# Optimization experiments

Hardware: AMD Instinct MI355X
Metric: run time of the kernel (lower is better)

## Reference

```python
import jax, jax.numpy as jnp
import numpy as np

B, T, E, H = 2, 4096, 1024, 16
SEGS = (256, 512, 1024, 2048, 4096)
DILS = (1, 2, 4, 8, 16)
NEG = -1e8  # torchscale uses -1e8 for uncovered / masked lse entries


def setup_inputs() -> dict:
    key = jax.random.key(0)
    ks = jax.random.split(key, 5)
    sc = 0.02
    zb = jnp.zeros((E,), jnp.float32)
    return {
        "x": jax.random.normal(ks[0], (B, T, E), jnp.float32),
        "wq": jax.random.normal(ks[1], (E, E), jnp.float32) * sc,
        "bq": zb,
        "wk": jax.random.normal(ks[2], (E, E), jnp.float32) * sc,
        "bk": zb,
        "wv": jax.random.normal(ks[3], (E, E), jnp.float32) * sc,
        "bv": zb,
        "wo": jax.random.normal(ks[4], (E, E), jnp.float32) * sc,
        "bo": zb,
    }


def _scale_attn(q, k, v, w, r):
    # One LongNet scale: segment length w, dilation ratio r.
    # Head group g = head // (H//r) attends to in-segment positions p with p % r == g
    # (torchscale dense_to_sparse diagonal over (r1, r2)).
    Bq, Tq, Hq, d = q.shape
    n, s, hp = Tq // w, w // r, Hq // r  # segments, sparse length, heads per group

    def gather(x):
        # [B,T,H,d] -> segments [B,n,w,H,d]; split w=(s,r1) (p=l*r+r1) and H=(r2,hp);
        # keep diagonal r1 == r2.
        x = x.reshape(Bq, n, s, r, r, hp, d)
        x = jnp.diagonal(x, axis1=3, axis2=4)          # [B,n,s,hp,d,r]
        return jnp.moveaxis(x, -1, 3).reshape(Bq, n, s, Hq, d)

    qs, ks_, vs = gather(q), gather(k), gather(v)
    scores = jnp.einsum('bnqhd,bnkhd->bnhqk', qs, ks_)
    mask = jnp.tril(jnp.ones((s, s), dtype=bool))       # causal within sparse segment
    scores = jnp.where(mask, scores, NEG)
    lse = jax.scipy.special.logsumexp(scores, axis=-1)  # [B,n,h,q]
    out = jnp.einsum('bnhqk,bnkhd->bnqhd', jax.nn.softmax(scores, axis=-1), vs)

    # Scatter back to dense positions (sparse_to_dense): uncovered -> out 0, lse -1e8.
    eye = jnp.eye(r, dtype=out.dtype)
    out_g = out.reshape(Bq, n, s, r, hp, d)                               # heads as (g, hp)
    dense = jnp.einsum('bnsghd,pg->bnspghd', out_g, eye).reshape(Bq, Tq, Hq, d)
    lse_g = jnp.transpose(lse, (0, 1, 3, 2)).reshape(Bq, n, s, r, hp)     # [B,n,s,g,hp]
    lse_d = jnp.where(eye[:, :, None] > 0, lse_g[:, :, :, None, :, :], NEG)
    return dense, lse_d.reshape(Bq, Tq, Hq)


def reference(x, wq, bq, wk, bk, wv, bv, wo, bo):
    d = E // H
    q = (x @ wq + bq).reshape(B, T, H, d) * (d ** -0.5)
    k = (x @ wk + bk).reshape(B, T, H, d)
    v = (x @ wv + bv).reshape(B, T, H, d)
    outs, lses = [], []
    for w_, r_ in zip(SEGS, DILS):
        o, l = _scale_attn(q, k, v, w_, r_)
        outs.append(o)
        lses.append(l)
    # Merge scales with softmax over per-scale log-sum-exp (dense-attention equivalence).
    wgt = jax.nn.softmax(jnp.stack(lses), axis=0)[..., None]  # [S,B,T,H,1]
    y = jnp.sum(jnp.stack(outs) * wgt, axis=0).reshape(B, T, E)
    return y @ wo + bo
```

## Files before the change

kernel.cpp:

```cpp
#include <hip/hip_runtime.h>
#include <hip/hip_bf16.h>

typedef __bf16 bf16_t;
typedef __bf16 bf16x8 __attribute__((ext_vector_type(8)));
typedef __bf16 bf16x4 __attribute__((ext_vector_type(4)));
typedef float f32x4 __attribute__((ext_vector_type(4)));
typedef int vint4 __attribute__((ext_vector_type(4)));

#define AS1 __attribute__((address_space(1)))
#define AS3 __attribute__((address_space(3)))

constexpr int B_ = 2, T_ = 4096, E_ = 1024, H_ = 16;
constexpr int M_ = B_ * T_;

__device__ constexpr size_t OB_OFF[5]  = {0, 8388608, 12582912, 14680064, 15728640};
__device__ constexpr size_t LSE_OFF[5] = {0, 131072, 196608, 229376, 245760};
constexpr size_t OB_TOTAL  = 16252928;
constexpr size_t LSE_TOTAL = 253952;

__global__ __launch_bounds__(256) void cvt_f32_bf16(const float* __restrict__ in,
                                                    bf16_t* __restrict__ out) {
  int i = (blockIdx.x * 256 + threadIdx.x) * 4;
  const float4 v = *(const float4*)(in + i);
  bf16x4 o;
  o[0] = (bf16_t)v.x; o[1] = (bf16_t)v.y; o[2] = (bf16_t)v.z; o[3] = (bf16_t)v.w;
  *(bf16x4*)(out + i) = o;
}

__global__ __launch_bounds__(256) void cvt_transpose_w(
    const float* __restrict__ w0, const float* __restrict__ w1,
    const float* __restrict__ w2, const float* __restrict__ w3,
    bf16_t* __restrict__ o0, bf16_t* __restrict__ o1,
    bf16_t* __restrict__ o2, bf16_t* __restrict__ o3) {
  __shared__ float tile[32][33];
  const float* src; bf16_t* dst;
  switch (blockIdx.z) {
    case 0: src = w0; dst = o0; break;
    case 1: src = w1; dst = o1; break;
    case 2: src = w2; dst = o2; break;
    default: src = w3; dst = o3; break;
  }
  const int n0 = blockIdx.x * 32, k0 = blockIdx.y * 32;
  const int tx = threadIdx.x & 31, ty = threadIdx.x >> 5;
#pragma unroll
  for (int i = 0; i < 32; i += 8)
    tile[ty + i][tx] = src[(size_t)(k0 + ty + i) * E_ + n0 + tx];
  __syncthreads();
#pragma unroll
  for (int i = 0; i < 32; i += 8)
    dst[(size_t)(n0 + ty + i) * E_ + k0 + tx] = (bf16_t)tile[tx][ty + i];
}

template <bool OUT_BF16, bool QKV>
__global__ __launch_bounds__(512, 1) void gemm_dp(
    const bf16_t* __restrict__ A, const bf16_t* __restrict__ BT,
    const float* __restrict__ bias0, const float* __restrict__ bias1,
    const float* __restrict__ bias2, void* __restrict__ Cout) {
  constexpr int K = E_;
  constexpr int NT = K / 64;
  __shared__ bf16_t Sm[73728];

  const int tid = threadIdx.x;
  const int lane = tid & 63;
  const int wid = tid >> 6;
  const int wm = wid >> 1, wn = wid & 1;
  const int lc = lane & 15, lg = lane >> 4;
  const int bm = blockIdx.x;
  int bn = blockIdx.y;

  const float* bias = bias0;
  float scale = 1.0f;
  void* outp = Cout;
  const bf16_t* Bt = BT;
  if (QKV) {
    const int which = bn >> 3;
    bn &= 7;
    bias = (which == 0) ? bias0 : (which == 1) ? bias1 : bias2;
    scale = (which == 0) ? 0.125f : 1.0f;
    outp = (void*)((bf16_t*)Cout + (size_t)which * M_ * E_);
    Bt += (size_t)which * E_ * E_;
  }

  const int srow = tid >> 3;
  const int schunk = (tid & 7) ^ (srow & 7);
  const bf16_t* Ag = A + (size_t)(bm * 256 + srow) * K + schunk * 8;
  const bf16_t* Bg = Bt + (size_t)(bn * 128 + srow) * K + schunk * 8;

  auto stA = [&](int kt, int bu) {
#pragma unroll
    for (int l = 0; l < 4; ++l)
      __builtin_amdgcn_global_load_lds(
          (const AS1 void*)(Ag + (size_t)(l * 64) * K + kt * 64),
          (AS3 void*)(Sm + bu * 16384 + l * 4096 + tid * 8), 16, 0, 0);
  };
  auto stB = [&](int kt, int bu) {
#pragma unroll
    for (int l = 0; l < 2; ++l)
      __builtin_amdgcn_global_load_lds(
          (const AS1 void*)(Bg + (size_t)(l * 64) * K + kt * 64),
          (AS3 void*)(Sm + 49152 + bu * 8192 + l * 4096 + tid * 8), 16, 0, 0);
  };

  const int sl0 = ((lg) ^ (lc & 7)) * 8;
  const int sl1 = ((4 + lg) ^ (lc & 7)) * 8;

  f32x4 acc[4][4] = {};

  stA(0, 0); stB(0, 0);
  stA(1, 1); stB(1, 1);

  for (int kt = 0; kt < NT; ++kt) {
    const int bc = kt % 3;
    if (kt + 2 < NT) {
      const int bs = (kt + 2) % 3;
      stA(kt + 2, bs); stB(kt + 2, bs);
      asm volatile("s_waitcnt vmcnt(12)" ::: "memory");
    } else if (kt + 1 < NT) {
      asm volatile("s_waitcnt vmcnt(6)" ::: "memory");
    } else {
      asm volatile("s_waitcnt vmcnt(0)" ::: "memory");
    }
    __builtin_amdgcn_s_barrier();
    asm volatile("" ::: "memory");

    const int ab = bc * 16384 + (wm * 64 + lc) * 64;
    const int bb = 49152 + bc * 8192 + (wn * 64 + lc) * 64;
    bf16x8 afr[4][2], bfr[4][2];
#pragma unroll
    for (int i = 0; i < 4; ++i) {
      afr[i][0] = *(const bf16x8*)&Sm[ab + i * 1024 + sl0];
      afr[i][1] = *(const bf16x8*)&Sm[ab + i * 1024 + sl1];
    }
#pragma unroll
    for (int j = 0; j < 4; ++j) {
      bfr[j][0] = *(const bf16x8*)&Sm[bb + j * 1024 + sl0];
      bfr[j][1] = *(const bf16x8*)&Sm[bb + j * 1024 + sl1];
    }
#pragma unroll
    for (int i = 0; i < 4; ++i)
#pragma unroll
      for (int j = 0; j < 4; ++j) {
        acc[i][j] = __builtin_amdgcn_mfma_f32_16x16x32_bf16(afr[i][0], bfr[j][0], acc[i][j], 0, 0, 0);
        acc[i][j] = __builtin_amdgcn_mfma_f32_16x16x32_bf16(afr[i][1], bfr[j][1], acc[i][j], 0, 0, 0);
      }
    asm volatile("" ::: "memory");
    __builtin_amdgcn_s_barrier();
  }

#pragma unroll
  for (int i = 0; i < 4; ++i) {
    const int row = bm * 256 + wm * 64 + i * 16 + lg * 4;
#pragma unroll
    for (int j = 0; j < 4; ++j) {
      const int col = bn * 128 + wn * 64 + j * 16 + lc;
      const float bv = bias[col];
#pragma unroll
      for (int rg = 0; rg < 4; ++rg) {
        const float v = (acc[i][j][rg] + bv) * scale;
        if (OUT_BF16)
          ((bf16_t*)outp)[(size_t)(row + rg) * E_ + col] = (bf16_t)v;
        else
          ((float*)outp)[(size_t)(row + rg) * E_ + col] = v;
      }
    }
  }
}

__global__ __launch_bounds__(512, 4) void attn_inst(
    const bf16_t* __restrict__ Q, const bf16_t* __restrict__ K,
    const bf16_t* __restrict__ V, bf16_t* __restrict__ Ob,
    float* __restrict__ Lse) {
  __shared__ alignas(16) bf16_t Ks[256][72];
  __shared__ alignas(16) bf16_t Vt[64][264];
  __shared__ alignas(16) bf16_t Pw[8][16][40];

  const int bid = blockIdx.x;
  int s, ibase;
  if (bid < 512)      { s = 0; ibase = 0; }
  else if (bid < 768) { s = 1; ibase = 512; }
  else if (bid < 896) { s = 2; ibase = 768; }
  else if (bid < 960) { s = 3; ibase = 896; }
  else                { s = 4; ibase = 960; }
  const int inst = bid - ibase;
  const int h = inst & 15;
  const int nseg_log = 4 - s;
  const int seg = (inst >> 4) & ((1 << nseg_log) - 1);
  const int b = inst >> (4 + nseg_log);
  const int g = h >> (4 - s);

  const int t = threadIdx.x;
  const int lane = t & 63;
  const int wv = t >> 6;
  const int lc = lane & 15;
  const int lg = lane >> 4;

  {
    const int row = t >> 1, ch = (t & 1) * 32;
    const int tk = ((seg * 256 + row) << s) + g;
    const size_t off = ((size_t)b * T_ + tk) * E_ + h * 64 + ch;
    const bf16_t* Kg = K + off;
    const bf16_t* Vg = V + off;
#pragma unroll
    for (int j = 0; j < 4; ++j)
      *(bf16x8*)&Ks[row][ch + j * 8] = *(const bf16x8*)(Kg + j * 8);
#pragma unroll
    for (int j = 0; j < 4; ++j) {
      bf16x8 va = *(const bf16x8*)(Vg + j * 8);
#pragma unroll
      for (int e = 0; e < 8; ++e) Vt[ch + j * 8 + e][row] = va[e];
    }
  }
  __syncthreads();

  const size_t rowbase = (size_t)(b * H_ + h) * (T_ >> s) + seg * 256;

#pragma unroll
  for (int sel = 0; sel < 2; ++sel) {
    const int tile = sel ? (15 - wv) : wv;
    const int q = tile * 16 + lc;

    const int tq = ((seg * 256 + q) << s) + g;
    const bf16_t* Qg = Q + ((size_t)b * T_ + tq) * E_ + h * 64 + lg * 8;
    bf16x8 qfrag0 = *(const bf16x8*)(Qg);
    bf16x8 qfrag1 = *(const bf16x8*)(Qg + 32);

    float m = -INFINITY, Z = 0.0f;
    f32x4 Oa[4] = {};

    const int nkb = tile / 4 + 1;
    const int diag = tile / 4;
    for (int kb = 0; kb < nkb; ++kb) {
      f32x4 sacc[4] = {};
      __builtin_amdgcn_s_setprio(1);
#pragma unroll
      for (int kt = 0; kt < 4; ++kt) {
        bf16x8 kf0 = *(const bf16x8*)&Ks[kb * 64 + kt * 16 + lc][lg * 8];
        bf16x8 kf1 = *(const bf16x8*)&Ks[kb * 64 + kt * 16 + lc][32 + lg * 8];
        sacc[kt] = __builtin_amdgcn_mfma_f32_16x16x32_bf16(kf0, qfrag0, sacc[kt], 0, 0, 0);
        sacc[kt] = __builtin_amdgcn_mfma_f32_16x16x32_bf16(kf1, qfrag1, sacc[kt], 0, 0, 0);
      }
      __builtin_amdgcn_s_setprio(0);
      if (kb == diag) {
#pragma unroll
        for (int kt = 0; kt < 4; ++kt)
#pragma unroll
          for (int rg = 0; rg < 4; ++rg)
            if (kb * 64 + kt * 16 + lg * 4 + rg > q) sacc[kt][rg] = -1e30f;
      }
      float pm = -1e30f;
#pragma unroll
      for (int kt = 0; kt < 4; ++kt) {
        pm = fmaxf(pm, fmaxf(fmaxf(sacc[kt][0], sacc[kt][1]),
                             fmaxf(sacc[kt][2], sacc[kt][3])));
      }
      pm = fmaxf(pm, __shfl_xor(pm, 16));
      pm = fmaxf(pm, __shfl_xor(pm, 32));
      const float nm = fmaxf(m, pm);
      const float crr = __expf(m - nm);
      m = nm;
      float psum = 0.0f;
      bf16x4 pv[4];
#pragma unroll
      for (int kt = 0; kt < 4; ++kt)
#pragma unroll
        for (int rg = 0; rg < 4; ++rg) {
          const float p = __expf(sacc[kt][rg] - nm);
          psum += p;
          pv[kt][rg] = (bf16_t)p;
        }
      psum += __shfl_xor(psum, 16);
      psum += __shfl_xor(psum, 32);
      Z = Z * crr + psum;
#pragma unroll
      for (int dt = 0; dt < 4; ++dt)
#pragma unroll
        for (int rg = 0; rg < 4; ++rg) Oa[dt][rg] *= crr;
#pragma unroll
      for (int hf = 0; hf < 2; ++hf) {
        *(bf16x4*)&Pw[wv][lc][lg * 4]      = pv[hf * 2 + 0];
        *(bf16x4*)&Pw[wv][lc][16 + lg * 4] = pv[hf * 2 + 1];
        bf16x8 pb = *(const bf16x8*)&Pw[wv][lc][lg * 8];
        __builtin_amdgcn_s_setprio(1);
#pragma unroll
        for (int dt = 0; dt < 4; ++dt) {
          bf16x8 vf = *(const bf16x8*)&Vt[dt * 16 + lc][(kb * 2 + hf) * 32 + lg * 8];
          Oa[dt] = __builtin_amdgcn_mfma_f32_16x16x32_bf16(vf, pb, Oa[dt], 0, 0, 0);
        }
        __builtin_amdgcn_s_setprio(0);
      }
    }

    const float lse = m + __logf(Z);
    const float iZ = 1.0f / Z;
    bf16_t* orow = Ob + OB_OFF[s] + (rowbase + q) * 64 + lg * 4;
#pragma unroll
    for (int dt = 0; dt < 4; ++dt) {
      bf16x4 ov;
      ov[0] = (bf16_t)(Oa[dt][0] * iZ);
      ov[1] = (bf16_t)(Oa[dt][1] * iZ);
      ov[2] = (bf16_t)(Oa[dt][2] * iZ);
      ov[3] = (bf16_t)(Oa[dt][3] * iZ);
      *(bf16x4*)(orow + dt * 16) = ov;
    }
    if (lg == 0) Lse[LSE_OFF[s] + rowbase + q] = lse;
  }
}

__global__ __launch_bounds__(256) void attn_merge(const bf16_t* __restrict__ Ob,
                                                  const float* __restrict__ Lse,
                                                  bf16_t* __restrict__ Y) {
  const int gtid = blockIdx.x * 256 + threadIdx.x;
  const int d8 = gtid & 7;
  const int h = (gtid >> 3) & 15;
  const int tt = (gtid >> 7) & (T_ - 1);
  const int b = gtid >> 19;

  float m = -INFINITY, S = 0.0f;
  float acc[8];
#pragma unroll
  for (int j = 0; j < 8; ++j) acc[j] = 0.0f;

#pragma unroll
  for (int s = 0; s < 5; ++s) {
    const int r = 1 << s;
    const int g = h >> (4 - s);
    if ((tt & (r - 1)) != g) continue;
    const size_t idx = (size_t)(b * H_ + h) * (T_ >> s) + (tt >> s);
    const float lse = Lse[LSE_OFF[s] + idx];
    const bf16x8 ov = *(const bf16x8*)(Ob + OB_OFF[s] + idx * 64 + d8 * 8);
    const float nM = fmaxf(m, lse);
    const float a = __expf(m - nM);
    const float e = __expf(lse - nM);
#pragma unroll
    for (int j = 0; j < 8; ++j) acc[j] = acc[j] * a + (float)ov[j] * e;
    S = S * a + e;
    m = nM;
  }

  const float invS = 1.0f / S;
  bf16x8 o;
#pragma unroll
  for (int j = 0; j < 8; ++j) o[j] = (bf16_t)(acc[j] * invS);
  *(bf16x8*)(Y + (size_t)gtid * 8) = o;
}

extern "C" void kernel_launch(void* const* d_in, const int* in_sizes, int n_in,
                              void* d_out, int out_size, void* d_ws, size_t ws_size,
                              hipStream_t stream) {
  (void)in_sizes; (void)n_in; (void)out_size; (void)ws_size;
  const float* x  = (const float*)d_in[0];
  const float* wq = (const float*)d_in[1];
  const float* bq = (const float*)d_in[2];
  const float* wk = (const float*)d_in[3];
  const float* bk = (const float*)d_in[4];
  const float* wv = (const float*)d_in[5];
  const float* bv = (const float*)d_in[6];
  const float* wo = (const float*)d_in[7];
  const float* bo = (const float*)d_in[8];

  char* p = (char*)d_ws;
  auto take = [&](size_t bytes) {
    char* q = p;
    p += (bytes + 255) & ~(size_t)255;
    return (void*)q;
  };
  bf16_t* wq_t = (bf16_t*)take((size_t)E_ * E_ * 2);
  bf16_t* wk_t = (bf16_t*)take((size_t)E_ * E_ * 2);
  bf16_t* wv_t = (bf16_t*)take((size_t)E_ * E_ * 2);
  bf16_t* wo_t = (bf16_t*)take((size_t)E_ * E_ * 2);
  bf16_t* xb   = (bf16_t*)take((size_t)M_ * E_ * 2);
  bf16_t* qb   = (bf16_t*)take((size_t)M_ * E_ * 2);
  bf16_t* kbuf = (bf16_t*)take((size_t)M_ * E_ * 2);
  bf16_t* vbuf = (bf16_t*)take((size_t)M_ * E_ * 2);
  bf16_t* yb   = (bf16_t*)take((size_t)M_ * E_ * 2);
  bf16_t* Ob   = (bf16_t*)take(OB_TOTAL * 2);
  float*  Lse  = (float*)take(LSE_TOTAL * 4);
  (void)wk_t; (void)wv_t;

  cvt_f32_bf16<<<M_ * E_ / 1024, 256, 0, stream>>>(x, xb);
  cvt_transpose_w<<<dim3(32, 32, 4), 256, 0, stream>>>(wq, wk, wv, wo, wq_t, wk_t, wv_t, wo_t);

  gemm_dp<true, true><<<dim3(M_ / 256, 24), 512, 0, stream>>>(
      xb, wq_t, bq, bk, bv, qb);

  attn_inst<<<992, 512, 0, stream>>>(qb, kbuf, vbuf, Ob, Lse);

  attn_merge<<<M_ * E_ / 8 / 256, 256, 0, stream>>>(Ob, Lse, yb);

  gemm_dp<false, false><<<dim3(M_ / 256, 8), 512, 0, stream>>>(
      yb, wo_t, bo, bo, bo, d_out);
}
```

Before: 138.0 us.

## Shrink GEMM tiles, fold log2e into Q scale, add lazy softmax rescaling

Replaces the 256x128 triple-buffered GEMM with a simpler 128x128 tile kernel of 256 threads and no prefetching, allowing up to 4 blocks per CU instead of one large block. Folds log2(e) into the Q scale so attention and merge use exp2/log2 instead of exp/log. Adds a wave-uniform threshold check that skips the running-max rescale of the accumulators when the new block max stays within a bound. The GEMM loses its software pipeline, and the lazy rescale lets exponent values grow before renormalisation.

```diff
diff --git a/kernel.cpp b/kernel.cpp
--- a/kernel.cpp
+++ b/kernel.cpp
@@ -52,18 +52,17 @@
 }
 
 template <bool OUT_BF16, bool QKV>
-__global__ __launch_bounds__(512, 1) void gemm_dp(
+__global__ __launch_bounds__(256, 4) void gemm_bt(
     const bf16_t* __restrict__ A, const bf16_t* __restrict__ BT,
     const float* __restrict__ bias0, const float* __restrict__ bias1,
-    const float* __restrict__ bias2, void* __restrict__ Cout) {
+    const float* __restrict__ bias2, void* __restrict__ Cout, float qscale) {
   constexpr int K = E_;
-  constexpr int NT = K / 64;
-  __shared__ bf16_t Sm[73728];
-
+  __shared__ bf16_t As[128 * 64];
+  __shared__ bf16_t Bs[128 * 64];
   const int tid = threadIdx.x;
   const int lane = tid & 63;
-  const int wid = tid >> 6;
-  const int wm = wid >> 1, wn = wid & 1;
+  const int wave = tid >> 6;
+  const int wm = wave >> 1, wn = wave & 1;
   const int lc = lane & 15, lg = lane >> 4;
   const int bm = blockIdx.x;
   int bn = blockIdx.y;
@@ -76,80 +75,53 @@
     const int which = bn >> 3;
     bn &= 7;
     bias = (which == 0) ? bias0 : (which == 1) ? bias1 : bias2;
-    scale = (which == 0) ? 0.125f : 1.0f;
+    scale = (which == 0) ? qscale : 1.0f;
     outp = (void*)((bf16_t*)Cout + (size_t)which * M_ * E_);
     Bt += (size_t)which * E_ * E_;
   }
 
-  const int srow = tid >> 3;
-  const int schunk = (tid & 7) ^ (srow & 7);
-  const bf16_t* Ag = A + (size_t)(bm * 256 + srow) * K + schunk * 8;
-  const bf16_t* Bg = Bt + (size_t)(bn * 128 + srow) * K + schunk * 8;
-
-  auto stA = [&](int kt, int bu) {
-#pragma unroll
-    for (int l = 0; l < 4; ++l)
+  f32x4 acc[4][4] = {};
+
+  const int lrow = tid >> 3;
+  const int schunk = (tid & 7) ^ (lrow & 7);
+  const bf16_t* Ag = A + (size_t)(bm * 128 + lrow) * K + schunk * 8;
+  const bf16_t* Bg = Bt + (size_t)(bn * 128 + lrow) * K + schunk * 8;
+
+  const int sl0 = ((0 * 4 + lg) ^ (lc & 7)) * 8;
+  const int sl1 = ((1 * 4 + lg) ^ (lc & 7)) * 8;
+
+  for (int k0 = 0; k0 < K; k0 += 64) {
+    __syncthreads();
+#pragma unroll
+    for (int p = 0; p < 4; ++p) {
       __builtin_amdgcn_global_load_lds(
-          (const AS1 void*)(Ag + (size_t)(l * 64) * K + kt * 64),
-          (AS3 void*)(Sm + bu * 16384 + l * 4096 + tid * 8), 16, 0, 0);
-  };
-  auto stB = [&](int kt, int bu) {
-#pragma unroll
-    for (int l = 0; l < 2; ++l)
+          (const AS1 void*)(Ag + (size_t)(p * 32) * K + k0),
+          (AS3 void*)(As + p * 2048 + tid * 8), 16, 0, 0);
       __builtin_amdgcn_global_load_lds(
-          (const AS1 void*)(Bg + (size_t)(l * 64) * K + kt * 64),
-          (AS3 void*)(Sm + 49152 + bu * 8192 + l * 4096 + tid * 8), 16, 0, 0);
-  };
-
-  const int sl0 = ((lg) ^ (lc & 7)) * 8;
-  const int sl1 = ((4 + lg) ^ (lc & 7)) * 8;
-
-  f32x4 acc[4][4] = {};
-
-  stA(0, 0); stB(0, 0);
-  stA(1, 1); stB(1, 1);
-
-  for (int kt = 0; kt < NT; ++kt) {
-    const int bc = kt % 3;
-    if (kt + 2 < NT) {
-      const int bs = (kt + 2) % 3;
-      stA(kt + 2, bs); stB(kt + 2, bs);
-      asm volatile("s_waitcnt vmcnt(12)" ::: "memory");
-    } else if (kt + 1 < NT) {
-      asm volatile("s_waitcnt vmcnt(6)" ::: "memory");
-    } else {
-      asm volatile("s_waitcnt vmcnt(0)" ::: "memory");
-    }
-    __builtin_amdgcn_s_barrier();
-    asm volatile("" ::: "memory");
-
-    const int ab = bc * 16384 + (wm * 64 + lc) * 64;
-    const int bb = 49152 + bc * 8192 + (wn * 64 + lc) * 64;
-    bf16x8 afr[4][2], bfr[4][2];
-#pragma unroll
-    for (int i = 0; i < 4; ++i) {
-      afr[i][0] = *(const bf16x8*)&Sm[ab + i * 1024 + sl0];
-      afr[i][1] = *(const bf16x8*)&Sm[ab + i * 1024 + sl1];
-    }
-#pragma unroll
-    for (int j = 0; j < 4; ++j) {
-      bfr[j][0] = *(const bf16x8*)&Sm[bb + j * 1024 + sl0];
-      bfr[j][1] = *(const bf16x8*)&Sm[bb + j * 1024 + sl1];
-    }
-#pragma unroll
-    for (int i = 0; i < 4; ++i)
-#pragma unroll
-      for (int j = 0; j < 4; ++j) {
-        acc[i][j] = __builtin_amdgcn_mfma_f32_16x16x32_bf16(afr[i][0], bfr[j][0], acc[i][j], 0, 0, 0);
-        acc[i][j] = __builtin_amdgcn_mfma_f32_16x16x32_bf16(afr[i][1], bfr[j][1], acc[i][j], 0, 0, 0);
-      }
-    asm volatile("" ::: "memory");
-    __builtin_amdgcn_s_barrier();
+          (const AS1 void*)(Bg + (size_t)(p * 32) * K + k0),
+          (AS3 void*)(Bs + p * 2048 + tid * 8), 16, 0, 0);
+    }
+    __syncthreads();
+#pragma unroll
+    for (int kk = 0; kk < 2; ++kk) {
+      const int sl = kk ? sl1 : sl0;
+      bf16x8 af[4], bfr[4];
+#pragma unroll
+      for (int i = 0; i < 4; ++i) {
+        af[i]  = *(const bf16x8*)&As[(wm * 64 + i * 16 + lc) * 64 + sl];
+        bfr[i] = *(const bf16x8*)&Bs[(wn * 64 + i * 16 + lc) * 64 + sl];
+      }
+#pragma unroll
+      for (int i = 0; i < 4; ++i)
+#pragma unroll
+        for (int j = 0; j < 4; ++j)
+          acc[i][j] = __builtin_amdgcn_mfma_f32_16x16x32_bf16(af[i], bfr[j], acc[i][j], 0, 0, 0);
+    }
   }
 
 #pragma unroll
   for (int i = 0; i < 4; ++i) {
-    const int row = bm * 256 + wm * 64 + i * 16 + lg * 4;
+    const int row = bm * 128 + wm * 64 + i * 16 + lg * 4;
 #pragma unroll
     for (int j = 0; j < 4; ++j) {
       const int col = bn * 128 + wn * 64 + j * 16 + lc;
@@ -255,26 +227,29 @@
       }
       pm = fmaxf(pm, __shfl_xor(pm, 16));
       pm = fmaxf(pm, __shfl_xor(pm, 32));
-      const float nm = fmaxf(m, pm);
-      const float crr = __expf(m - nm);
-      m = nm;
+      if (!__all(pm - m <= 11.5f)) {
+        const float nm = fmaxf(m, pm);
+        const float crr = exp2f(m - nm);
+        Z *= crr;
+#pragma unroll
+        for (int dt = 0; dt < 4; ++dt)
+#pragma unroll
+          for (int rg = 0; rg < 4; ++rg) Oa[dt][rg] *= crr;
+        m = nm;
+      }
       float psum = 0.0f;
       bf16x4 pv[4];
 #pragma unroll
       for (int kt = 0; kt < 4; ++kt)
 #pragma unroll
         for (int rg = 0; rg < 4; ++rg) {
-          const float p = __expf(sacc[kt][rg] - nm);
+          const float p = exp2f(sacc[kt][rg] - m);
           psum += p;
           pv[kt][rg] = (bf16_t)p;
         }
       psum += __shfl_xor(psum, 16);
       psum += __shfl_xor(psum, 32);
-      Z = Z * crr + psum;
-#pragma unroll
-      for (int dt = 0; dt < 4; ++dt)
-#pragma unroll
-        for (int rg = 0; rg < 4; ++rg) Oa[dt][rg] *= crr;
+      Z += psum;
 #pragma unroll
       for (int hf = 0; hf < 2; ++hf) {
         *(bf16x4*)&Pw[wv][lc][lg * 4]      = pv[hf * 2 + 0];
@@ -290,7 +265,7 @@
       }
     }
 
-    const float lse = m + __logf(Z);
+    const float lse = m + log2f(Z);
     const float iZ = 1.0f / Z;
     bf16_t* orow = Ob + OB_OFF[s] + (rowbase + q) * 64 + lg * 4;
 #pragma unroll
@@ -329,8 +304,8 @@
     const float lse = Lse[LSE_OFF[s] + idx];
     const bf16x8 ov = *(const bf16x8*)(Ob + OB_OFF[s] + idx * 64 + d8 * 8);
     const float nM = fmaxf(m, lse);
-    const float a = __expf(m - nM);
-    const float e = __expf(lse - nM);
+    const float a = exp2f(m - nM);
+    const float e = exp2f(lse - nM);
 #pragma unroll
     for (int j = 0; j < 8; ++j) acc[j] = acc[j] * a + (float)ov[j] * e;
     S = S * a + e;
@@ -380,13 +355,13 @@
   cvt_f32_bf16<<<M_ * E_ / 1024, 256, 0, stream>>>(x, xb);
   cvt_transpose_w<<<dim3(32, 32, 4), 256, 0, stream>>>(wq, wk, wv, wo, wq_t, wk_t, wv_t, wo_t);
 
-  gemm_dp<true, true><<<dim3(M_ / 256, 24), 512, 0, stream>>>(
-      xb, wq_t, bq, bk, bv, qb);
+  gemm_bt<true, true><<<dim3(M_ / 128, 24), 256, 0, stream>>>(
+      xb, wq_t, bq, bk, bv, qb, 0.125f * 1.44269504f);
 
   attn_inst<<<992, 512, 0, stream>>>(qb, kbuf, vbuf, Ob, Lse);
 
   attn_merge<<<M_ * E_ / 8 / 256, 256, 0, stream>>>(Ob, Lse, yb);
 
-  gemm_dp<false, false><<<dim3(M_ / 256, 8), 512, 0, stream>>>(
-      yb, wo_t, bo, bo, bo, d_out);
-}
+  gemm_bt<false, false><<<dim3(M_ / 128, 8), 256, 0, stream>>>(
+      yb, wo_t, bo, bo, bo, d_out, 1.0f);
+}
```

Result: faster. 133.3 us (-3.4%).
